# Kernel tuning notes

Hardware: AMD Instinct MI355X
Metric: run time of the kernel (lower is better)

The kernel has to match this reference:

```python
import jax, jax.numpy as jnp
import numpy as np

UF = 4  # upscale_factor; pixel_shuffle factor hardcoded to 4 in the original


def setup_inputs() -> dict:
    key = jax.random.key(0)
    pic_in = jax.random.normal(key, (32, 400, 1, 1, 64, 64), dtype=jnp.float32)
    return {"pic_in": pic_in}


def reference(pic_in):
    # pic_in: [B, C=400, d2, d3, H, W]; only [:, :, 0, 0] is read.
    B, C, _, _, H, W = pic_in.shape
    r = UF
    c_out = C // (r * r)  # 25
    x = pic_in[:, :, 0, 0, :, :]                       # [B, 400, H, W]
    # torch.pixel_shuffle: out[c, h*r+i, w*r+j] = in[c*r*r + i*r + j, h, w]
    x = x.reshape(B, c_out, r, r, H, W)
    x = x.transpose(0, 1, 4, 2, 5, 3)                  # [B, 25, H, r, W, r]
    x = x.reshape(B, c_out, H * r, W * r)              # [B, 25, 4H, 4W]
    # slicing upscaled[i*5:i*5+5] into out[:, i] == reshape 25 -> (5, 5)
    return x.reshape(B, 5, 5, H * r, W * r)
```

## Files before the change

### kernel.cpp

```cpp
#include <hip/hip_runtime.h>


#define CH_PAD 17

__global__ __launch_bounds__(256) void recon_ps4_lds_kernel(
    const float* __restrict__ in, float* __restrict__ out)
{
    __shared__ float lds[4 * 64 * CH_PAD];

    const int blk = blockIdx.x;
    const int h4  = blk & 15;
    const int bc  = blk >> 4;

    const int td  = threadIdx.x;
    const int ch  = td >> 4;
    const int l16 = td & 15;

    const float* src = in + ((size_t)(bc * 16 + ch) * 4096 + (size_t)h4 * 256 + l16 * 4);
    float4 v0 = *reinterpret_cast<const float4*>(src);
    float4 v1 = *reinterpret_cast<const float4*>(src + 64);
    float4 v2 = *reinterpret_cast<const float4*>(src + 128);
    float4 v3 = *reinterpret_cast<const float4*>(src + 192);

    const int w0 = l16 * 4;
    float* p0 = lds + (0 * 64 + w0) * CH_PAD + ch;
    float* p1 = lds + (1 * 64 + w0) * CH_PAD + ch;
    float* p2 = lds + (2 * 64 + w0) * CH_PAD + ch;
    float* p3 = lds + (3 * 64 + w0) * CH_PAD + ch;
    p0[0] = v0.x; p0[CH_PAD] = v0.y; p0[2*CH_PAD] = v0.z; p0[3*CH_PAD] = v0.w;
    p1[0] = v1.x; p1[CH_PAD] = v1.y; p1[2*CH_PAD] = v1.z; p1[3*CH_PAD] = v1.w;
    p2[0] = v2.x; p2[CH_PAD] = v2.y; p2[2*CH_PAD] = v2.z; p2[3*CH_PAD] = v2.w;
    p3[0] = v3.x; p3[CH_PAD] = v3.y; p3[2*CH_PAD] = v3.z; p3[3*CH_PAD] = v3.w;

    __syncthreads();

    float* dst = out + ((size_t)bc * 65536 + (size_t)h4 * 4096);
    const int i  = td >> 6;
    const int w  = td & 63;

    #pragma unroll
    for (int q = 0; q < 4; ++q) {
        float4 r = *reinterpret_cast<const float4*>(lds + (q * 64 + w) * CH_PAD + i * 4);
        *reinterpret_cast<float4*>(dst + q * 1024 + td * 4) = r;
    }
}

extern "C" void kernel_launch(void* const* d_in, const int* in_sizes, int n_in,
                              void* d_out, int out_size, void* d_ws, size_t ws_size,
                              hipStream_t stream) {
    const float* in = (const float*)d_in[0];
    float* out = (float*)d_out;

    recon_ps4_lds_kernel<<<12800, 256, 0, stream>>>(in, out);
}
```

Baseline: 78.90 us.

## Use direct global-to-LDS loads and process four row groups per block

Replaces register-staged loads plus padded LDS transposes with global_load_lds DMA writes straight into shared memory. Each block now loops over four row-groups, which cuts the grid to a quarter of its former size. Each wave waits on its own vmcnt rather than a block barrier, because every wave reads only the LDS region it filled. The unpadded layout may bring LDS bank conflicts on reads, and the serialized per-iteration waits may reduce memory-level parallelism.

```diff
diff --git a/kernel.cpp b/kernel.cpp
--- a/kernel.cpp
+++ b/kernel.cpp
@@ -1,47 +1,57 @@
 #include <hip/hip_runtime.h>
 
 
-#define CH_PAD 17
+#define AS_GLOBAL __attribute__((address_space(1)))
+#define AS_LOCAL  __attribute__((address_space(3)))
 
-__global__ __launch_bounds__(256) void recon_ps4_lds_kernel(
+__global__ __launch_bounds__(256) void recon_ps4_dma(
     const float* __restrict__ in, float* __restrict__ out)
 {
-    __shared__ float lds[4 * 64 * CH_PAD];
+    __shared__ float lds[4096];
 
-    const int blk = blockIdx.x;
-    const int h4  = blk & 15;
-    const int bc  = blk >> 4;
+    const int td   = threadIdx.x;
+    const int wid  = td >> 6;
+    const int lane = td & 63;
+    const int ch   = td >> 4;
+    const int l16  = td & 15;
 
-    const int td  = threadIdx.x;
-    const int ch  = td >> 4;
-    const int l16 = td & 15;
+    const int g  = blockIdx.x & 3;
+    const int bc = blockIdx.x >> 2;
 
-    const float* src = in + ((size_t)(bc * 16 + ch) * 4096 + (size_t)h4 * 256 + l16 * 4);
-    float4 v0 = *reinterpret_cast<const float4*>(src);
-    float4 v1 = *reinterpret_cast<const float4*>(src + 64);
-    float4 v2 = *reinterpret_cast<const float4*>(src + 128);
-    float4 v3 = *reinterpret_cast<const float4*>(src + 192);
-
-    const int w0 = l16 * 4;
-    float* p0 = lds + (0 * 64 + w0) * CH_PAD + ch;
-    float* p1 = lds + (1 * 64 + w0) * CH_PAD + ch;
-    float* p2 = lds + (2 * 64 + w0) * CH_PAD + ch;
-    float* p3 = lds + (3 * 64 + w0) * CH_PAD + ch;
-    p0[0] = v0.x; p0[CH_PAD] = v0.y; p0[2*CH_PAD] = v0.z; p0[3*CH_PAD] = v0.w;
-    p1[0] = v1.x; p1[CH_PAD] = v1.y; p1[2*CH_PAD] = v1.z; p1[3*CH_PAD] = v1.w;
-    p2[0] = v2.x; p2[CH_PAD] = v2.y; p2[2*CH_PAD] = v2.z; p2[3*CH_PAD] = v2.w;
-    p3[0] = v3.x; p3[CH_PAD] = v3.y; p3[2*CH_PAD] = v3.z; p3[3*CH_PAD] = v3.w;
-
-    __syncthreads();
-
-    float* dst = out + ((size_t)bc * 65536 + (size_t)h4 * 4096);
-    const int i  = td >> 6;
-    const int w  = td & 63;
+    const float* src0 = in + ((size_t)(bc * 16 + ch) << 12)
+                           + (size_t)(g << 10) + (l16 << 2);
+    char* lds_dst = (char*)lds + (wid << 10) + (lane << 4);
+    const float* rbase = lds + (wid << 8) + lane;
+    float* dst0 = out + ((size_t)bc << 16) + ((size_t)g << 14);
 
     #pragma unroll
-    for (int q = 0; q < 4; ++q) {
-        float4 r = *reinterpret_cast<const float4*>(lds + (q * 64 + w) * CH_PAD + i * 4);
-        *reinterpret_cast<float4*>(dst + q * 1024 + td * 4) = r;
+    for (int it = 0; it < 4; ++it) {
+        const float* s = src0 + it * 256;
+
+        #pragma unroll
+        for (int hh = 0; hh < 4; ++hh) {
+            __builtin_amdgcn_global_load_lds(
+                (const AS_GLOBAL void*)(s + hh * 64),
+                (AS_LOCAL void*)(lds_dst + hh * 4096),
+                16, 0, 0);
+        }
+        asm volatile("s_waitcnt vmcnt(0)" ::: "memory");
+
+        float v[4][4];
+        #pragma unroll
+        for (int q = 0; q < 4; ++q)
+            #pragma unroll
+            for (int j = 0; j < 4; ++j)
+                v[q][j] = rbase[q * 1024 + j * 64];
+
+        asm volatile("s_waitcnt lgkmcnt(0)" ::: "memory");
+
+        float* d = dst0 + (it << 12) + (td << 2);
+        #pragma unroll
+        for (int q = 0; q < 4; ++q) {
+            float4 o = make_float4(v[q][0], v[q][1], v[q][2], v[q][3]);
+            *reinterpret_cast<float4*>(d + (q << 10)) = o;
+        }
     }
 }
 
@@ -51,5 +61,5 @@
     const float* in = (const float*)d_in[0];
     float* out = (float*)d_out;
 
-    recon_ps4_lds_kernel<<<12800, 256, 0, stream>>>(in, out);
+    recon_ps4_dma<<<3200, 256, 0, stream>>>(in, out);
 }
```

Result: slower. 88.05 us (+11.6%).

## Drop block barrier via wavefront-local LDS exchange, unpadded layout, nontemporal stores

Applied to the files above, without the earlier changes.

Reorganizes the LDS staging so each 64-thread wavefront reads back only the channels it wrote itself. This lets the kernel drop __syncthreads and rely on in-order LDS access within a wave. The padded layout is replaced by an unpadded one with vector writes and stride-64 scalar reads. Output stores become nontemporal to avoid polluting the cache. The change depends on a 64-wide wavefront and is limited by a kernel that is already close to memory bandwidth.

```diff
diff --git a/kernel.cpp b/kernel.cpp
--- a/kernel.cpp
+++ b/kernel.cpp
@@ -1,47 +1,43 @@
 #include <hip/hip_runtime.h>
 
 
-#define CH_PAD 17
+typedef float vfloat4 __attribute__((ext_vector_type(4)));
 
-__global__ __launch_bounds__(256) void recon_ps4_lds_kernel(
+__global__ __launch_bounds__(256) void recon_ps4(
     const float* __restrict__ in, float* __restrict__ out)
 {
-    __shared__ float lds[4 * 64 * CH_PAD];
-
-    const int blk = blockIdx.x;
-    const int h4  = blk & 15;
-    const int bc  = blk >> 4;
+    __shared__ float lds[4096];
 
     const int td  = threadIdx.x;
+    const int wid = td >> 6;
+    const int w   = td & 63;
     const int ch  = td >> 4;
     const int l16 = td & 15;
 
-    const float* src = in + ((size_t)(bc * 16 + ch) * 4096 + (size_t)h4 * 256 + l16 * 4);
-    float4 v0 = *reinterpret_cast<const float4*>(src);
-    float4 v1 = *reinterpret_cast<const float4*>(src + 64);
-    float4 v2 = *reinterpret_cast<const float4*>(src + 128);
-    float4 v3 = *reinterpret_cast<const float4*>(src + 192);
+    const int h4 = blockIdx.x & 15;
+    const int bc = blockIdx.x >> 4;
 
-    const int w0 = l16 * 4;
-    float* p0 = lds + (0 * 64 + w0) * CH_PAD + ch;
-    float* p1 = lds + (1 * 64 + w0) * CH_PAD + ch;
-    float* p2 = lds + (2 * 64 + w0) * CH_PAD + ch;
-    float* p3 = lds + (3 * 64 + w0) * CH_PAD + ch;
-    p0[0] = v0.x; p0[CH_PAD] = v0.y; p0[2*CH_PAD] = v0.z; p0[3*CH_PAD] = v0.w;
-    p1[0] = v1.x; p1[CH_PAD] = v1.y; p1[2*CH_PAD] = v1.z; p1[3*CH_PAD] = v1.w;
-    p2[0] = v2.x; p2[CH_PAD] = v2.y; p2[2*CH_PAD] = v2.z; p2[3*CH_PAD] = v2.w;
-    p3[0] = v3.x; p3[CH_PAD] = v3.y; p3[2*CH_PAD] = v3.z; p3[3*CH_PAD] = v3.w;
+    const float* src = in + ((size_t)(bc * 16 + ch) << 12) + (h4 << 8) + (l16 << 2);
+    vfloat4 v[4];
+    #pragma unroll
+    for (int hh = 0; hh < 4; ++hh)
+        v[hh] = *reinterpret_cast<const vfloat4*>(src + (hh << 6));
 
-    __syncthreads();
+    float* wp = lds + (ch << 6) + (l16 << 2);
+    #pragma unroll
+    for (int hh = 0; hh < 4; ++hh)
+        *reinterpret_cast<vfloat4*>(wp + (hh << 10)) = v[hh];
 
-    float* dst = out + ((size_t)bc * 65536 + (size_t)h4 * 4096);
-    const int i  = td >> 6;
-    const int w  = td & 63;
-
+    const float* rb = lds + (wid << 8) + w;
+    float* dst = out + ((size_t)bc << 16) + (h4 << 12) + (wid << 8) + (w << 2);
     #pragma unroll
     for (int q = 0; q < 4; ++q) {
-        float4 r = *reinterpret_cast<const float4*>(lds + (q * 64 + w) * CH_PAD + i * 4);
-        *reinterpret_cast<float4*>(dst + q * 1024 + td * 4) = r;
+        vfloat4 o;
+        o.x = rb[(q << 10)      ];
+        o.y = rb[(q << 10) +  64];
+        o.z = rb[(q << 10) + 128];
+        o.w = rb[(q << 10) + 192];
+        __builtin_nontemporal_store(o, reinterpret_cast<vfloat4*>(dst + (q << 10)));
     }
 }
 
@@ -51,5 +47,5 @@
     const float* in = (const float*)d_in[0];
     float* out = (float*)d_out;
 
-    recon_ps4_lds_kernel<<<12800, 256, 0, stream>>>(in, out);
+    recon_ps4<<<12800, 256, 0, stream>>>(in, out);
 }
```

Result: faster. 66.92 us (-15.2%).
